# Performance work log

Measured on AMD Instinct MI355X. Metric: run time of the kernel, lower is better.

The kernel has to match this reference:

```python
import jax, jax.numpy as jnp
import numpy as np

B, N, D, H, DK, DV, R = 4, 256, 256, 8, 32, 32, 64
EPS = 1e-6


def setup_inputs() -> dict:
    key = jax.random.key(0)
    ks = jax.random.split(key, 16)
    s = D ** -0.5
    return {
        "q": jax.random.normal(ks[0], (B, N, D), jnp.float32),
        "k": jax.random.normal(ks[1], (B, N, D), jnp.float32),
        "v": jax.random.normal(ks[2], (B, N, D), jnp.float32),
        "mask": jax.random.randint(ks[3], (B, N, N), 0, 2).astype(jnp.int32),
        "link": jax.random.uniform(ks[4], (B, N, N, R), jnp.float32),
        "Wq": jax.random.normal(ks[5], (D, H * DK), jnp.float32) * s,
        "Wk": jax.random.normal(ks[6], (D, H * DK), jnp.float32) * s,
        "Wr": jax.random.normal(ks[7], (D, H * DK), jnp.float32) * s,
        "Wv": jax.random.normal(ks[8], (D, H * DV), jnp.float32) * s,
        "Wvv": jax.random.normal(ks[9], (D, H * DV), jnp.float32) * s,
        "relationE": jax.random.normal(ks[10], (R, D), jnp.float32) * s,
        "Wo": jax.random.normal(ks[11], (H * DV, D), jnp.float32) * s,
        "gamma": jnp.ones((D,), jnp.float32),
        "beta": jnp.zeros((D,), jnp.float32),
    }


def reference(q, k, v, mask, link, Wq, Wk, Wr, Wv, Wvv, relationE, Wo, gamma, beta):
    # rela_num != 0 branch of Ruleformer MultiHeadAttention (dropout = identity, eval mode).
    residual = q
    b, n, d = q.shape
    # per-head projections of X (== q == residual in this branch): [b,h,n,dk]
    Xq = (q @ Wq).reshape(b, n, H, DK).transpose(0, 2, 1, 3)
    Xk = (q @ Wk).reshape(b, n, H, DK).transpose(0, 2, 1, 3)
    Xv = (q @ Wv).reshape(b, n, H, DV).transpose(0, 2, 1, 3)

    # calcE: relation-biased scores. Rk[b,i,j,h,d] = (link @ relationE @ Wr)
    Rk = jnp.einsum('bijr,re->bije', link, relationE @ Wr).reshape(b, n, n, H, DK)
    # attn[b,h,i,j] = Xq[b,h,i] . (Xk[b,h,j] + Rk[b,i,j,h])
    attn = jnp.einsum('bhid,bhjd->bhij', Xq, Xk)
    attn = attn + jnp.einsum('bijhd,bhid->bhij', Rk, Xq)
    attn = attn / (DK ** 0.5)
    attn = jnp.where(mask[:, None, :, :] == 0, -1e9, attn)
    alpha = jax.nn.softmax(attn, axis=-1)  # [b,h,n,n]

    # calcZ: Z[b,h,i] = sum_j alpha[b,h,i,j] * (Xv[b,h,j] + Rv[b,i,j,h])
    Rv = jnp.einsum('bijr,re->bije', link, relationE @ Wvv).reshape(b, n, n, H, DV)
    Z = jnp.einsum('bhij,bhjd->bhid', alpha, Xv)
    Z = Z + jnp.einsum('bhij,bijhd->bhid', alpha, Rv)

    out = Z.transpose(0, 2, 1, 3).reshape(b, n, H * DV) @ Wo
    out = out + residual
    mu = out.mean(-1, keepdims=True)
    var = ((out - mu) ** 2).mean(-1, keepdims=True)
    out = (out - mu) * jax.lax.rsqrt(var + EPS) * gamma + beta
    return out, alpha
```

## Files before the change

### kernel.cpp

```cpp
#include <hip/hip_runtime.h>
#include <math.h>

constexpr int B_ = 4, N_ = 256, D_ = 256, H_ = 8, DK_ = 32, DV_ = 32, R_ = 64;
constexpr float SCALE_ = 0.17677669529663687f;
constexpr float EPS_ = 1e-6f;

__global__ __launch_bounds__(256) void ekev_kernel(
        const float* __restrict__ relE, const float* __restrict__ Wr,
        const float* __restrict__ Wvv, float* __restrict__ Ek,
        float* __restrict__ Ev) {
    int r = blockIdx.x & 63;
    int which = blockIdx.x >> 6;
    const float* W = which ? Wvv : Wr;
    float* out = which ? Ev : Ek;
    __shared__ float row[256];
    int tid = threadIdx.x;
    row[tid] = relE[r * 256 + tid];
    __syncthreads();
    float acc = 0.f;
    for (int d = 0; d < 256; ++d) acc += row[d] * W[d * 256 + tid];
    out[r * 256 + tid] = acc;
}

__global__ __launch_bounds__(256) void mcat_kernel(
        const float* __restrict__ Wq, const float* __restrict__ Ek,
        float* __restrict__ M) {
    int d = blockIdx.x;
    int t = threadIdx.x;
    __shared__ float wrow[256];
    wrow[t] = Wq[d * 256 + t];
    __syncthreads();
    for (int hr = t; hr < 512; hr += 256) {
        int h = hr >> 6, r = hr & 63;
        const float4* ek4 = (const float4*)(Ek + r * 256 + h * 32);
        const float4* w4 = (const float4*)(wrow + h * 32);
        float acc = 0.f;
#pragma unroll
        for (int k = 0; k < 8; ++k) {
            float4 e = ek4[k], w = w4[k];
            acc += e.x * w.x + e.y * w.y + e.z * w.z + e.w * w.w;
        }
        M[d * 512 + hr] = acc;
    }
}

__global__ __launch_bounds__(256) void projT_kernel(
        const float* __restrict__ q, const float* __restrict__ Wq,
        const float* __restrict__ Wk, const float* __restrict__ Wv,
        const float* __restrict__ M, float* __restrict__ Xq,
        float* __restrict__ Xk, float* __restrict__ Xv,
        float* __restrict__ T) {
    int ct = blockIdx.x >> 4, rt = blockIdx.x & 15;
    int t = threadIdx.x;
    __shared__ float ash[32 * 65];
    __shared__ float bsh[32 * 64];
    const float* W;
    int ncols, cbase;
    if (ct < 4)       { W = Wq; cbase = ct * 64;        ncols = 256; }
    else if (ct < 8)  { W = Wk; cbase = (ct - 4) * 64;  ncols = 256; }
    else if (ct < 12) { W = Wv; cbase = (ct - 8) * 64;  ncols = 256; }
    else              { W = M;  cbase = (ct - 12) * 64; ncols = 512; }
    int ti = t >> 4, tj = t & 15;
    float acc[4][4] = {{0.f}};
    for (int kc = 0; kc < 8; ++kc) {
        __syncthreads();
#pragma unroll
        for (int kk = 0; kk < 2; ++kk) {
            int m = t + kk * 256;
            int i = m >> 3, kq = m & 7;
            float4 v = *(const float4*)(q + (size_t)(rt * 64 + i) * 256 + kc * 32 + kq * 4);
            ash[(kq * 4 + 0) * 65 + i] = v.x;
            ash[(kq * 4 + 1) * 65 + i] = v.y;
            ash[(kq * 4 + 2) * 65 + i] = v.z;
            ash[(kq * 4 + 3) * 65 + i] = v.w;
        }
#pragma unroll
        for (int kk = 0; kk < 2; ++kk) {
            int m = t + kk * 256;
            int k = m >> 4, j4 = m & 15;
            float4 v = *(const float4*)(W + (size_t)(kc * 32 + k) * ncols + cbase + j4 * 4);
            *(float4*)(bsh + k * 64 + j4 * 4) = v;
        }
        __syncthreads();
#pragma unroll 8
        for (int k = 0; k < 32; ++k) {
            float4 av = *(const float4*)(ash + k * 65 + ti * 4);
            float4 bv = *(const float4*)(bsh + k * 64 + tj * 4);
            acc[0][0] += av.x * bv.x; acc[0][1] += av.x * bv.y;
            acc[0][2] += av.x * bv.z; acc[0][3] += av.x * bv.w;
            acc[1][0] += av.y * bv.x; acc[1][1] += av.y * bv.y;
            acc[1][2] += av.y * bv.z; acc[1][3] += av.y * bv.w;
            acc[2][0] += av.z * bv.x; acc[2][1] += av.z * bv.y;
            acc[2][2] += av.z * bv.z; acc[2][3] += av.z * bv.w;
            acc[3][0] += av.w * bv.x; acc[3][1] += av.w * bv.y;
            acc[3][2] += av.w * bv.z; acc[3][3] += av.w * bv.w;
        }
    }
    if (ct < 12) {
        float* dst = (ct < 4) ? Xq : (ct < 8) ? Xk : Xv;
        int gcol = (ct & 3) * 64 + tj * 4;
        int h = gcol >> 5, dk = gcol & 31;
#pragma unroll
        for (int a = 0; a < 4; ++a) {
            int row = rt * 64 + ti * 4 + a;
            int bb = row >> 8, n = row & 255;
            *(float4*)(dst + ((size_t)(bb * 8 + h) * 256 + n) * 32 + dk) =
                make_float4(acc[a][0], acc[a][1], acc[a][2], acc[a][3]);
        }
    } else {
        int gcol = (ct - 12) * 64 + tj * 4;
#pragma unroll
        for (int a = 0; a < 4; ++a) {
            int row = rt * 64 + ti * 4 + a;
            *(float4*)(T + (size_t)row * 512 + gcol) =
                make_float4(acc[a][0], acc[a][1], acc[a][2], acc[a][3]);
        }
    }
}

__global__ __launch_bounds__(256) void qk_kernel(
        const float* __restrict__ Xq, const float* __restrict__ Xk,
        float* __restrict__ qk) {
    int x = blockIdx.x;
    int jt = x & 3, it = (x >> 2) & 3, bh = x >> 4;
    int t = threadIdx.x;
    __shared__ float xqsh[32 * 64];
    __shared__ float xksh[32 * 64];
#pragma unroll
    for (int k = 0; k < 2; ++k) {
        int m = t + k * 256;
        int i = m >> 3, dq4 = m & 7;
        float4 v = *(const float4*)(Xq + ((size_t)(bh * 256 + it * 64 + i)) * 32 + dq4 * 4);
        xqsh[(dq4 * 4 + 0) * 64 + i] = v.x;
        xqsh[(dq4 * 4 + 1) * 64 + i] = v.y;
        xqsh[(dq4 * 4 + 2) * 64 + i] = v.z;
        xqsh[(dq4 * 4 + 3) * 64 + i] = v.w;
        float4 u = *(const float4*)(Xk + ((size_t)(bh * 256 + jt * 64 + i)) * 32 + dq4 * 4);
        xksh[(dq4 * 4 + 0) * 64 + i] = u.x;
        xksh[(dq4 * 4 + 1) * 64 + i] = u.y;
        xksh[(dq4 * 4 + 2) * 64 + i] = u.z;
        xksh[(dq4 * 4 + 3) * 64 + i] = u.w;
    }
    __syncthreads();
    int ti = t >> 4, tj = t & 15;
    float acc[4][4] = {{0.f}};
#pragma unroll 8
    for (int dk = 0; dk < 32; ++dk) {
        float4 av = *(const float4*)(xqsh + dk * 64 + ti * 4);
        float4 bv = *(const float4*)(xksh + dk * 64 + tj * 4);
        acc[0][0] += av.x * bv.x; acc[0][1] += av.x * bv.y;
        acc[0][2] += av.x * bv.z; acc[0][3] += av.x * bv.w;
        acc[1][0] += av.y * bv.x; acc[1][1] += av.y * bv.y;
        acc[1][2] += av.y * bv.z; acc[1][3] += av.y * bv.w;
        acc[2][0] += av.z * bv.x; acc[2][1] += av.z * bv.y;
        acc[2][2] += av.z * bv.z; acc[2][3] += av.z * bv.w;
        acc[3][0] += av.w * bv.x; acc[3][1] += av.w * bv.y;
        acc[3][2] += av.w * bv.z; acc[3][3] += av.w * bv.w;
    }
#pragma unroll
    for (int a = 0; a < 4; ++a) {
        int i = it * 64 + ti * 4 + a;
        *(float4*)(qk + ((size_t)(bh * 256 + i)) * 256 + jt * 64 + tj * 4) =
            make_float4(acc[a][0], acc[a][1], acc[a][2], acc[a][3]);
    }
}

__global__ __launch_bounds__(256) void biassm_kernel(
        const float* __restrict__ link, const float* __restrict__ Tg,
        const float* __restrict__ qk, const int* __restrict__ mask,
        float* __restrict__ alpha, float* __restrict__ S) {
    int bi = blockIdx.x;
    int b = bi >> 8, i = bi & 255;
    int t = threadIdx.x;
    __shared__ float4 linksh4[64 * 16];
    __shared__ float Tsh[512];
    __shared__ float ashm[2048];
    __shared__ float part[2048];
    __shared__ float redsh[64];
    Tsh[t] = Tg[(size_t)bi * 512 + t];
    Tsh[256 + t] = Tg[(size_t)bi * 512 + 256 + t];

    for (int c = 0; c < 4; ++c) {
        __syncthreads();
        {
            const float4* lp = (const float4*)(link + ((size_t)(bi * 256 + c * 64)) * 64);
#pragma unroll
            for (int k = 0; k < 4; ++k) {
                int m = t + k * 256;
                int j = m >> 4, rq = m & 15;
                linksh4[j * 16 + (rq ^ (j & 15))] = lp[m];
            }
        }
        __syncthreads();
        int j = t & 63, rg = t >> 6;
        float pacc[8] = {0.f, 0.f, 0.f, 0.f, 0.f, 0.f, 0.f, 0.f};
#pragma unroll
        for (int rq = 0; rq < 4; ++rq) {
            int r0 = rg * 16 + rq * 4;
            float4 lv = linksh4[j * 16 + ((rg * 4 + rq) ^ (j & 15))];
#pragma unroll
            for (int h = 0; h < 8; ++h) {
                float4 tv = *(const float4*)(Tsh + h * 64 + r0);
                pacc[h] += lv.x * tv.x + lv.y * tv.y + lv.z * tv.z + lv.w * tv.w;
            }
        }
#pragma unroll
        for (int h = 0; h < 8; ++h) part[rg * 512 + h * 64 + j] = pacc[h];
        __syncthreads();
        if ((t >> 6) == c) {
            int jj = t & 63;
#pragma unroll
            for (int h = 0; h < 8; ++h)
                ashm[h * 256 + t] = part[h * 64 + jj] + part[512 + h * 64 + jj] +
                                    part[1024 + h * 64 + jj] + part[1536 + h * 64 + jj];
        }
    }
    __syncthreads();

    int j = t;
    float s[8];
#pragma unroll
    for (int h = 0; h < 8; ++h) {
        size_t off = ((size_t)(b * 8 + h) * 256 + i) * 256 + j;
        s[h] = (qk[off] + ashm[h * 256 + j]) * SCALE_;
    }
    if (mask[(b * 256 + i) * 256 + j] == 0) {
#pragma unroll
        for (int h = 0; h < 8; ++h) s[h] = -1e9f;
    }
    int lane = t & 63, wv = t >> 6;
#pragma unroll
    for (int h = 0; h < 8; ++h) {
        float v = s[h];
        for (int off = 32; off > 0; off >>= 1) v = fmaxf(v, __shfl_xor(v, off));
        if (lane == 0) redsh[h * 4 + wv] = v;
    }
    __syncthreads();
    float mx[8];
#pragma unroll
    for (int h = 0; h < 8; ++h)
        mx[h] = fmaxf(fmaxf(redsh[h * 4 + 0], redsh[h * 4 + 1]),
                      fmaxf(redsh[h * 4 + 2], redsh[h * 4 + 3]));
    __syncthreads();
#pragma unroll
    for (int h = 0; h < 8; ++h) {
        float e = __expf(s[h] - mx[h]);
        s[h] = e;
        float v = e;
        for (int off = 32; off > 0; off >>= 1) v += __shfl_xor(v, off);
        if (lane == 0) redsh[32 + h * 4 + wv] = v;
    }
    __syncthreads();
#pragma unroll
    for (int h = 0; h < 8; ++h) {
        float esum = redsh[32 + h * 4 + 0] + redsh[32 + h * 4 + 1] +
                     redsh[32 + h * 4 + 2] + redsh[32 + h * 4 + 3];
        float a = s[h] * (1.f / esum);
        ashm[h * 256 + j] = a;
        alpha[((size_t)(b * 8 + h) * 256 + i) * 256 + j] = a;
    }
    __syncthreads();

    int r = t & 63, g = t >> 6;
    float pacc2[8] = {0.f, 0.f, 0.f, 0.f, 0.f, 0.f, 0.f, 0.f};
    const float* lp2 = link + ((size_t)(bi * 256 + g * 64)) * 64 + r;
#pragma unroll 4
    for (int j4 = 0; j4 < 16; ++j4) {
        float l0 = lp2[(j4 * 4 + 0) * 64];
        float l1 = lp2[(j4 * 4 + 1) * 64];
        float l2 = lp2[(j4 * 4 + 2) * 64];
        float l3 = lp2[(j4 * 4 + 3) * 64];
#pragma unroll
        for (int h = 0; h < 8; ++h) {
            float4 a = *(const float4*)(ashm + h * 256 + g * 64 + j4 * 4);
            pacc2[h] += a.x * l0 + a.y * l1 + a.z * l2 + a.w * l3;
        }
    }
#pragma unroll
    for (int h = 0; h < 8; ++h) part[g * 512 + h * 64 + r] = pacc2[h];
    __syncthreads();
    for (int hr = t; hr < 512; hr += 256) {
        S[(size_t)bi * 512 + hr] =
            part[hr] + part[512 + hr] + part[1024 + hr] + part[1536 + hr];
    }
}

__global__ __launch_bounds__(256) void zout_kernel(
        const float* __restrict__ alpha, const float* __restrict__ Xv,
        const float* __restrict__ S, const float* __restrict__ Ev,
        const float* __restrict__ Wo, const float* __restrict__ q,
        const float* __restrict__ gamma, const float* __restrict__ beta,
        float* __restrict__ out) {
    int blk = blockIdx.x;
    int row0 = blk * 2;
    int b = row0 >> 8;
    int t = threadIdx.x;
    __shared__ float Ssh[2 * 512];
    __shared__ float ashm[2 * 2048];
    __shared__ float zsh[2 * 256];
    __shared__ float redsh[16];
    for (int m = t; m < 1024; m += 256)
        Ssh[m] = S[(size_t)(row0 + (m >> 9)) * 512 + (m & 511)];
    for (int m = t; m < 4096; m += 256) {
        int rr = m >> 11, h = (m >> 8) & 7, j = m & 255;
        ashm[m] = alpha[((size_t)(b * 8 + h) * 256 + ((row0 + rr) & 255)) * 256 + j];
    }
    __syncthreads();
    {
        int h = t >> 5, dv = t & 31;
        float z0 = 0.f, z1 = 0.f;
        const float* xv = Xv + ((size_t)(b * 8 + h) * 256) * 32 + dv;
#pragma unroll 4
        for (int j = 0; j < 256; ++j) {
            float x = xv[j * 32];
            z0 += ashm[h * 256 + j] * x;
            z1 += ashm[2048 + h * 256 + j] * x;
        }
#pragma unroll 4
        for (int r = 0; r < 64; ++r) {
            float ev = Ev[r * 256 + h * 32 + dv];
            z0 += Ssh[h * 64 + r] * ev;
            z1 += Ssh[512 + h * 64 + r] * ev;
        }
        zsh[t] = z0;
        zsh[256 + t] = z1;
    }
    __syncthreads();
    float a0 = q[(size_t)row0 * 256 + t];
    float a1 = q[(size_t)(row0 + 1) * 256 + t];
    for (int d4 = 0; d4 < 64; ++d4) {
        float w0 = Wo[(d4 * 4 + 0) * 256 + t];
        float w1 = Wo[(d4 * 4 + 1) * 256 + t];
        float w2 = Wo[(d4 * 4 + 2) * 256 + t];
        float w3 = Wo[(d4 * 4 + 3) * 256 + t];
        float4 z0v = *(const float4*)(zsh + d4 * 4);
        float4 z1v = *(const float4*)(zsh + 256 + d4 * 4);
        a0 += z0v.x * w0 + z0v.y * w1 + z0v.z * w2 + z0v.w * w3;
        a1 += z1v.x * w0 + z1v.y * w1 + z1v.z * w2 + z1v.w * w3;
    }
    int lane = t & 63, wv = t >> 6;
    float acc2[2] = {a0, a1};
#pragma unroll
    for (int rr = 0; rr < 2; ++rr) {
        float v = acc2[rr], v2 = acc2[rr] * acc2[rr];
        for (int off = 32; off > 0; off >>= 1) {
            v += __shfl_xor(v, off);
            v2 += __shfl_xor(v2, off);
        }
        if (lane == 0) {
            redsh[rr * 8 + wv] = v;
            redsh[rr * 8 + 4 + wv] = v2;
        }
    }
    __syncthreads();
#pragma unroll
    for (int rr = 0; rr < 2; ++rr) {
        float sum = redsh[rr * 8 + 0] + redsh[rr * 8 + 1] + redsh[rr * 8 + 2] + redsh[rr * 8 + 3];
        float sum2 = redsh[rr * 8 + 4] + redsh[rr * 8 + 5] + redsh[rr * 8 + 6] + redsh[rr * 8 + 7];
        float mu = sum * (1.f / 256.f);
        float var = sum2 * (1.f / 256.f) - mu * mu;
        float dev = acc2[rr] - mu;
        out[(size_t)(row0 + rr) * 256 + t] = dev * rsqrtf(var + EPS_) * gamma[t] + beta[t];
    }
}

extern "C" void kernel_launch(void* const* d_in, const int* in_sizes, int n_in,
                              void* d_out, int out_size, void* d_ws, size_t ws_size,
                              hipStream_t stream) {
    const float* q     = (const float*)d_in[0];
    const int*   mask  = (const int*)d_in[3];
    const float* link  = (const float*)d_in[4];
    const float* Wq    = (const float*)d_in[5];
    const float* Wk    = (const float*)d_in[6];
    const float* Wr    = (const float*)d_in[7];
    const float* Wv    = (const float*)d_in[8];
    const float* Wvv   = (const float*)d_in[9];
    const float* relE  = (const float*)d_in[10];
    const float* Wo    = (const float*)d_in[11];
    const float* gamma = (const float*)d_in[12];
    const float* beta  = (const float*)d_in[13];

    float* out   = (float*)d_out;
    float* alpha = out + B_ * N_ * D_;

    float* ws    = (float*)d_ws;
    float* Ek    = ws;
    float* Ev    = Ek + 16384;
    float* Mcat  = Ev + 16384;
    float* Xq    = Mcat + 131072;
    float* Xk    = Xq + 262144;
    float* Xv    = Xk + 262144;
    float* T     = Xv + 262144;
    float* qkbuf = T + 524288;
    float* S     = qkbuf + 2097152;

    ekev_kernel<<<128, 256, 0, stream>>>(relE, Wr, Wvv, Ek, Ev);
    mcat_kernel<<<256, 256, 0, stream>>>(Wq, Ek, Mcat);
    projT_kernel<<<320, 256, 0, stream>>>(q, Wq, Wk, Wv, Mcat, Xq, Xk, Xv, T);
    qk_kernel<<<512, 256, 0, stream>>>(Xq, Xk, qkbuf);
    biassm_kernel<<<1024, 256, 0, stream>>>(link, T, qkbuf, mask, alpha, S);
    zout_kernel<<<512, 256, 0, stream>>>(alpha, Xv, S, Ev, Wo, q, gamma, beta, out);
}
```

Measured before the change: 204.2 us.

## Fuse QK scores into bias-softmax kernel and stage link once via async LDS copies

Removes the separate qk kernel and its 8 MB intermediate buffer by computing Xq·Xk dot products inside the bias/softmax kernel per (b,i) row. The full 64 KB link slice is now loaded once into shared memory with global_load_lds async copies (XOR-swizzled), overlapped with the QK dot products, and reused for both the score bias and the alpha·link reduction instead of being re-read from global. Block indices are permuted for locality, and one barrier is dropped. The 64 KB+ LDS footprint lowers occupancy, and the per-thread Xk reads are uncoalesced row reads.

```diff
diff --git a/kernel.cpp b/kernel.cpp
--- a/kernel.cpp
+++ b/kernel.cpp
@@ -118,122 +118,83 @@
     }
 }
 
-__global__ __launch_bounds__(256) void qk_kernel(
+__device__ __forceinline__ void async_cp16(void* lds, const void* g) {
+    __builtin_amdgcn_global_load_lds(
+        (const __attribute__((address_space(1))) void*)g,
+        (__attribute__((address_space(3))) void*)lds, 16, 0, 0);
+}
+
+__global__ __launch_bounds__(256) void biassmqk_kernel(
+        const float* __restrict__ link, const float* __restrict__ Tg,
         const float* __restrict__ Xq, const float* __restrict__ Xk,
-        float* __restrict__ qk) {
-    int x = blockIdx.x;
-    int jt = x & 3, it = (x >> 2) & 3, bh = x >> 4;
-    int t = threadIdx.x;
-    __shared__ float xqsh[32 * 64];
-    __shared__ float xksh[32 * 64];
-#pragma unroll
-    for (int k = 0; k < 2; ++k) {
-        int m = t + k * 256;
-        int i = m >> 3, dq4 = m & 7;
-        float4 v = *(const float4*)(Xq + ((size_t)(bh * 256 + it * 64 + i)) * 32 + dq4 * 4);
-        xqsh[(dq4 * 4 + 0) * 64 + i] = v.x;
-        xqsh[(dq4 * 4 + 1) * 64 + i] = v.y;
-        xqsh[(dq4 * 4 + 2) * 64 + i] = v.z;
-        xqsh[(dq4 * 4 + 3) * 64 + i] = v.w;
-        float4 u = *(const float4*)(Xk + ((size_t)(bh * 256 + jt * 64 + i)) * 32 + dq4 * 4);
-        xksh[(dq4 * 4 + 0) * 64 + i] = u.x;
-        xksh[(dq4 * 4 + 1) * 64 + i] = u.y;
-        xksh[(dq4 * 4 + 2) * 64 + i] = u.z;
-        xksh[(dq4 * 4 + 3) * 64 + i] = u.w;
-    }
-    __syncthreads();
-    int ti = t >> 4, tj = t & 15;
-    float acc[4][4] = {{0.f}};
-#pragma unroll 8
-    for (int dk = 0; dk < 32; ++dk) {
-        float4 av = *(const float4*)(xqsh + dk * 64 + ti * 4);
-        float4 bv = *(const float4*)(xksh + dk * 64 + tj * 4);
-        acc[0][0] += av.x * bv.x; acc[0][1] += av.x * bv.y;
-        acc[0][2] += av.x * bv.z; acc[0][3] += av.x * bv.w;
-        acc[1][0] += av.y * bv.x; acc[1][1] += av.y * bv.y;
-        acc[1][2] += av.y * bv.z; acc[1][3] += av.y * bv.w;
-        acc[2][0] += av.z * bv.x; acc[2][1] += av.z * bv.y;
-        acc[2][2] += av.z * bv.z; acc[2][3] += av.z * bv.w;
-        acc[3][0] += av.w * bv.x; acc[3][1] += av.w * bv.y;
-        acc[3][2] += av.w * bv.z; acc[3][3] += av.w * bv.w;
-    }
-#pragma unroll
-    for (int a = 0; a < 4; ++a) {
-        int i = it * 64 + ti * 4 + a;
-        *(float4*)(qk + ((size_t)(bh * 256 + i)) * 256 + jt * 64 + tj * 4) =
-            make_float4(acc[a][0], acc[a][1], acc[a][2], acc[a][3]);
-    }
-}
-
-__global__ __launch_bounds__(256) void biassm_kernel(
-        const float* __restrict__ link, const float* __restrict__ Tg,
-        const float* __restrict__ qk, const int* __restrict__ mask,
-        float* __restrict__ alpha, float* __restrict__ S) {
-    int bi = blockIdx.x;
+        const int* __restrict__ mask, float* __restrict__ alpha,
+        float* __restrict__ S) {
+    int bi = ((blockIdx.x & 7) << 7) | (blockIdx.x >> 3);
     int b = bi >> 8, i = bi & 255;
     int t = threadIdx.x;
-    __shared__ float4 linksh4[64 * 16];
-    __shared__ float Tsh[512];
-    __shared__ float ashm[2048];
-    __shared__ float part[2048];
-    __shared__ float redsh[64];
-    Tsh[t] = Tg[(size_t)bi * 512 + t];
-    Tsh[256 + t] = Tg[(size_t)bi * 512 + 256 + t];
-
-    for (int c = 0; c < 4; ++c) {
-        __syncthreads();
-        {
-            const float4* lp = (const float4*)(link + ((size_t)(bi * 256 + c * 64)) * 64);
-#pragma unroll
-            for (int k = 0; k < 4; ++k) {
-                int m = t + k * 256;
-                int j = m >> 4, rq = m & 15;
-                linksh4[j * 16 + (rq ^ (j & 15))] = lp[m];
+    int g = t >> 6, l = t & 63;
+    int j = g * 64 + l;
+
+    __shared__ float linksh[16384];
+    __shared__ float absh[2048];
+    __shared__ float uni[2048];
+
+    uni[t]       = Tg[(size_t)bi * 512 + t];
+    uni[256 + t] = Tg[(size_t)bi * 512 + 256 + t];
+    uni[512 + t] = Xq[(((size_t)(b * 8 + (t >> 5))) * 256 + i) * 32 + (t & 31)];
+    __syncthreads();
+
+    {
+        const float* gsrc = link + (((size_t)bi * 256 + g * 64) * 64);
+        float* ldst = linksh + g * 4096;
+        int jl = l >> 4, sl = l & 15;
+#pragma unroll
+        for (int k = 0; k < 16; ++k) {
+            int jj = k * 4 + jl;
+            int rq = sl ^ (jj & 15);
+            async_cp16(ldst + k * 256, gsrc + jj * 64 + rq * 4);
+        }
+    }
+    int mv = mask[((size_t)(b * 256 + i)) * 256 + j];
+
+    float s[8];
+#pragma unroll
+    for (int h = 0; h < 8; ++h) {
+        const float4* xk4 = (const float4*)(Xk + (((size_t)(b * 8 + h)) * 256 + j) * 32);
+        const float4* qx4 = (const float4*)(uni + 512 + h * 32);
+        float acc = 0.f;
+#pragma unroll
+        for (int kq = 0; kq < 8; ++kq) {
+            float4 xv = xk4[kq], qv = qx4[kq];
+            acc += xv.x * qv.x + xv.y * qv.y + xv.z * qv.z + xv.w * qv.w;
+        }
+        s[h] = acc;
+    }
+
+    asm volatile("s_waitcnt vmcnt(0)" ::: "memory");
+    __builtin_amdgcn_sched_barrier(0);
+    {
+        const float4* lk4 = ((const float4*)linksh) + g * 1024 + l * 16;
+        const float4* T4 = (const float4*)uni;
+#pragma unroll
+        for (int rq = 0; rq < 16; ++rq) {
+            float4 lv = lk4[rq ^ (l & 15)];
+#pragma unroll
+            for (int h = 0; h < 8; ++h) {
+                float4 tv = T4[h * 16 + rq];
+                s[h] += lv.x * tv.x + lv.y * tv.y + lv.z * tv.z + lv.w * tv.w;
             }
         }
-        __syncthreads();
-        int j = t & 63, rg = t >> 6;
-        float pacc[8] = {0.f, 0.f, 0.f, 0.f, 0.f, 0.f, 0.f, 0.f};
-#pragma unroll
-        for (int rq = 0; rq < 4; ++rq) {
-            int r0 = rg * 16 + rq * 4;
-            float4 lv = linksh4[j * 16 + ((rg * 4 + rq) ^ (j & 15))];
-#pragma unroll
-            for (int h = 0; h < 8; ++h) {
-                float4 tv = *(const float4*)(Tsh + h * 64 + r0);
-                pacc[h] += lv.x * tv.x + lv.y * tv.y + lv.z * tv.z + lv.w * tv.w;
-            }
-        }
-#pragma unroll
-        for (int h = 0; h < 8; ++h) part[rg * 512 + h * 64 + j] = pacc[h];
-        __syncthreads();
-        if ((t >> 6) == c) {
-            int jj = t & 63;
-#pragma unroll
-            for (int h = 0; h < 8; ++h)
-                ashm[h * 256 + t] = part[h * 64 + jj] + part[512 + h * 64 + jj] +
-                                    part[1024 + h * 64 + jj] + part[1536 + h * 64 + jj];
-        }
-    }
-    __syncthreads();
-
-    int j = t;
-    float s[8];
-#pragma unroll
-    for (int h = 0; h < 8; ++h) {
-        size_t off = ((size_t)(b * 8 + h) * 256 + i) * 256 + j;
-        s[h] = (qk[off] + ashm[h * 256 + j]) * SCALE_;
-    }
-    if (mask[(b * 256 + i) * 256 + j] == 0) {
-#pragma unroll
-        for (int h = 0; h < 8; ++h) s[h] = -1e9f;
-    }
-    int lane = t & 63, wv = t >> 6;
+    }
+#pragma unroll
+    for (int h = 0; h < 8; ++h) s[h] = (mv == 0) ? -1e9f : s[h] * SCALE_;
+
+    float* redsh = uni + 768;
 #pragma unroll
     for (int h = 0; h < 8; ++h) {
         float v = s[h];
         for (int off = 32; off > 0; off >>= 1) v = fmaxf(v, __shfl_xor(v, off));
-        if (lane == 0) redsh[h * 4 + wv] = v;
+        if (l == 0) redsh[h * 4 + g] = v;
     }
     __syncthreads();
     float mx[8];
@@ -241,14 +202,13 @@
     for (int h = 0; h < 8; ++h)
         mx[h] = fmaxf(fmaxf(redsh[h * 4 + 0], redsh[h * 4 + 1]),
                       fmaxf(redsh[h * 4 + 2], redsh[h * 4 + 3]));
-    __syncthreads();
 #pragma unroll
     for (int h = 0; h < 8; ++h) {
         float e = __expf(s[h] - mx[h]);
         s[h] = e;
         float v = e;
         for (int off = 32; off > 0; off >>= 1) v += __shfl_xor(v, off);
-        if (lane == 0) redsh[32 + h * 4 + wv] = v;
+        if (l == 0) redsh[32 + h * 4 + g] = v;
     }
     __syncthreads();
 #pragma unroll
@@ -256,32 +216,37 @@
         float esum = redsh[32 + h * 4 + 0] + redsh[32 + h * 4 + 1] +
                      redsh[32 + h * 4 + 2] + redsh[32 + h * 4 + 3];
         float a = s[h] * (1.f / esum);
-        ashm[h * 256 + j] = a;
+        absh[h * 256 + j] = a;
         alpha[((size_t)(b * 8 + h) * 256 + i) * 256 + j] = a;
     }
     __syncthreads();
 
-    int r = t & 63, g = t >> 6;
-    float pacc2[8] = {0.f, 0.f, 0.f, 0.f, 0.f, 0.f, 0.f, 0.f};
-    const float* lp2 = link + ((size_t)(bi * 256 + g * 64)) * 64 + r;
-#pragma unroll 4
-    for (int j4 = 0; j4 < 16; ++j4) {
-        float l0 = lp2[(j4 * 4 + 0) * 64];
-        float l1 = lp2[(j4 * 4 + 1) * 64];
-        float l2 = lp2[(j4 * 4 + 2) * 64];
-        float l3 = lp2[(j4 * 4 + 3) * 64];
-#pragma unroll
-        for (int h = 0; h < 8; ++h) {
-            float4 a = *(const float4*)(ashm + h * 256 + g * 64 + j4 * 4);
-            pacc2[h] += a.x * l0 + a.y * l1 + a.z * l2 + a.w * l3;
-        }
-    }
-#pragma unroll
-    for (int h = 0; h < 8; ++h) part[g * 512 + h * 64 + r] = pacc2[h];
-    __syncthreads();
-    for (int hr = t; hr < 512; hr += 256) {
-        S[(size_t)bi * 512 + hr] =
-            part[hr] + part[512 + hr] + part[1024 + hr] + part[1536 + hr];
+    {
+        const float* lks = linksh + g * 4096;
+        float pacc[8] = {0.f, 0.f, 0.f, 0.f, 0.f, 0.f, 0.f, 0.f};
+#pragma unroll
+        for (int j4 = 0; j4 < 16; ++j4) {
+            int j0 = j4 * 4;
+            float l0 = lks[(j0 + 0) * 64 + (l ^ (((j0 + 0) & 15) << 2))];
+            float l1 = lks[(j0 + 1) * 64 + (l ^ (((j0 + 1) & 15) << 2))];
+            float l2 = lks[(j0 + 2) * 64 + (l ^ (((j0 + 2) & 15) << 2))];
+            float l3 = lks[(j0 + 3) * 64 + (l ^ (((j0 + 3) & 15) << 2))];
+#pragma unroll
+            for (int h = 0; h < 8; ++h) {
+                float4 av = *(const float4*)(absh + h * 256 + g * 64 + j0);
+                pacc[h] += av.x * l0 + av.y * l1 + av.z * l2 + av.w * l3;
+            }
+        }
+        float* partS = uni;
+#pragma unroll
+        for (int h = 0; h < 8; ++h) partS[g * 512 + h * 64 + l] = pacc[h];
+    }
+    __syncthreads();
+    {
+        const float* partS = uni;
+        for (int hr = t; hr < 512; hr += 256)
+            S[(size_t)bi * 512 + hr] = partS[hr] + partS[512 + hr] +
+                                       partS[1024 + hr] + partS[1536 + hr];
     }
 }
 
@@ -391,13 +356,11 @@
     float* Xk    = Xq + 262144;
     float* Xv    = Xk + 262144;
     float* T     = Xv + 262144;
-    float* qkbuf = T + 524288;
-    float* S     = qkbuf + 2097152;
+    float* S     = T + 524288;
 
     ekev_kernel<<<128, 256, 0, stream>>>(relE, Wr, Wvv, Ek, Ev);
     mcat_kernel<<<256, 256, 0, stream>>>(Wq, Ek, Mcat);
     projT_kernel<<<320, 256, 0, stream>>>(q, Wq, Wk, Wv, Mcat, Xq, Xk, Xv, T);
-    qk_kernel<<<512, 256, 0, stream>>>(Xq, Xk, qkbuf);
-    biassm_kernel<<<1024, 256, 0, stream>>>(link, T, qkbuf, mask, alpha, S);
+    biassmqk_kernel<<<1024, 256, 0, stream>>>(link, T, Xq, Xk, mask, alpha, S);
     zout_kernel<<<512, 256, 0, stream>>>(alpha, Xv, S, Ev, Wo, q, gamma, beta, out);
 }
```

Measured after the change: 451.1 us. +120.9%, slower.
